# Kernel tuning notes

Hardware: AMD Instinct MI355X
Metric: run time of the kernel (lower is better)

Reference implementation:

```python
import jax, jax.numpy as jnp
import numpy as np

B, N, E, G, V = 8, 512, 8192, 1024, 100000
HD, FIN, BN_EPS = 1024, 20, 1e-5


def setup_inputs() -> dict:
    key = jax.random.key(0)
    ks = jax.random.split(key, 8)
    return {
        'h': jax.random.normal(ks[0], (B, N, FIN), jnp.float32),
        'src': jax.random.randint(ks[1], (B, E), 0, N, jnp.int32),
        'dst': jax.random.randint(ks[2], (B, E), 0, N, jnp.int32),
        'gPos': jax.random.randint(ks[3], (B, G), 0, V, jnp.int32),
        'allDBGEmb': jax.random.normal(ks[4], (V, HD), jnp.float32),
        'fc_init_w': jax.random.normal(ks[5], (HD, FIN), jnp.float32) * (1.0 / np.sqrt(FIN)),
        'fc_init_b': jnp.zeros((HD,), jnp.float32),
        'bn1_g': jnp.ones((HD,), jnp.float32),
        'bn1_b': jnp.zeros((HD,), jnp.float32),
        'bn2_g': jnp.ones((HD,), jnp.float32),
        'bn2_b': jnp.zeros((HD,), jnp.float32),
        'fc_w': jax.random.normal(ks[6], (128, 2 * HD), jnp.float32) * (1.0 / np.sqrt(2 * HD)),
        'fc_b': jnp.zeros((128,), jnp.float32),
        'bn3_g': jnp.ones((128,), jnp.float32),
        'bn3_b': jnp.zeros((128,), jnp.float32),
        'fc2_w': jax.random.normal(ks[7], (1, 128), jnp.float32) * (1.0 / np.sqrt(128)),
        'fc2_b': jnp.zeros((1,), jnp.float32),
    }


def _bn(x, g, b):
    # BatchNorm1d in training mode: batch statistics over axis 0 (biased var)
    mu = x.mean(0)
    var = ((x - mu) ** 2).mean(0)
    return (x - mu) * jax.lax.rsqrt(var + BN_EPS) * g + b


def _gin_mean(x, s, d):
    # GINConv(None, 'mean') with eps=0: h_v + mean_{u in N(v)} h_u
    sums = jax.ops.segment_sum(x[s], d, num_segments=N)  # [N, HD]
    deg = jax.ops.segment_sum(jnp.ones((E, 1), x.dtype), d, num_segments=N)
    return x + jnp.where(deg > 0, sums / jnp.maximum(deg, 1.0), 0.0)


def reference(h, src, dst, gPos, allDBGEmb, fc_init_w, fc_init_b,
              bn1_g, bn1_b, bn2_g, bn2_b, fc_w, fc_b, bn3_g, bn3_b,
              fc2_w, fc2_b):
    def per_graph(hq, s, d, gp):
        x = hq @ fc_init_w.T + fc_init_b                      # [N, HD]
        x = jax.nn.relu(_bn(_gin_mean(x, s, d), bn1_g, bn1_b))
        x = jax.nn.relu(_bn(_gin_mean(x, s, d), bn2_g, bn2_b))
        qemb = x.mean(0)                                      # dgl.mean_nodes
        gEmb = allDBGEmb[gp]                                  # [G, HD]
        H = jnp.concatenate([jnp.broadcast_to(qemb, (G, HD)), gEmb], axis=1)
        h2 = jax.nn.relu(_bn(H @ fc_w.T + fc_b, bn3_g, bn3_b))
        return jax.nn.sigmoid(h2 @ fc2_w.T + fc2_b).reshape(-1)  # [G]

    return jax.vmap(per_graph)(h, src, dst, gPos)  # [B, G]
```

## Files before the change

### kernel.cpp

```cpp
#include <hip/hip_runtime.h>
#include <hip/hip_bf16.h>

#define B_ 8
#define G_ 1024
#define HD_ 1024
#define EPS_ 1e-5f


typedef __attribute__((ext_vector_type(8))) short bf16x8;
typedef __attribute__((ext_vector_type(4))) float f32x4;

__device__ inline short bf1(float x) {
    return (short)__builtin_bit_cast(unsigned short, __float2bfloat16(x));
}
__device__ inline bf16x8 cvt8(float4 a, float4 b) {
    bf16x8 o;
    o[0] = bf1(a.x); o[1] = bf1(a.y); o[2] = bf1(a.z); o[3] = bf1(a.w);
    o[4] = bf1(b.x); o[5] = bf1(b.y); o[6] = bf1(b.z); o[7] = bf1(b.w);
    return o;
}

__global__ __launch_bounds__(256) void k_w2cvt(const float* __restrict__ fc_w,
                                               short* __restrict__ w2arr) {
    int gid = blockIdx.x * 256 + threadIdx.x;
    int kt = gid >> 9;
    int jblk = (gid >> 6) & 7;
    int lane = gid & 63;
    int j = jblk * 16 + (lane & 15);
    int k = kt * 32 + (lane >> 4) * 8;
    const float4* sp = (const float4*)&fc_w[(size_t)j * (2 * HD_) + HD_ + k];
    *(bf16x8*)&w2arr[(size_t)gid * 8] = cvt8(sp[0], sp[1]);
}

#define ASLAB 258

__global__ __launch_bounds__(512) void k_gemm(const int* __restrict__ gPos,
                                              const float* __restrict__ emb,
                                              const short* __restrict__ w2arr,
                                              float* __restrict__ z,
                                              float* __restrict__ ps,
                                              float* __restrict__ pq) {
    int b = blockIdx.y, gblk = blockIdx.x;
    int gbase = gblk * 32;
    int tid = threadIdx.x;
    int wave = tid >> 6, lane = tid & 63;
    int gq = wave >> 2, jq = wave & 3;
    int l15 = lane & 15, kb = lane >> 4;

    __shared__ int gidx[32];
    __shared__ short As[2][16 * ASLAB];

    if (tid < 32) gidx[tid] = gPos[b * G_ + gbase + tid];
    __syncthreads();

    int arow = tid >> 4, acp = tid & 15;
    const float* abase = emb + (size_t)gidx[arow] * HD_;

    f32x4 acc0 = {0.f, 0.f, 0.f, 0.f}, acc1 = {0.f, 0.f, 0.f, 0.f};

    {
        const float4* ap = (const float4*)(abase + acp * 8);
        *(bf16x8*)&As[0][acp * ASLAB + arow * 8] = cvt8(ap[0], ap[1]);
    }
    __syncthreads();

    for (int p = 0; p < 8; ++p) {
        int cur = p & 1;
        if (p < 7) {
            const float4* ap = (const float4*)(abase + (p + 1) * 128 + acp * 8);
            *(bf16x8*)&As[cur ^ 1][acp * ASLAB + arow * 8] = cvt8(ap[0], ap[1]);
        }
#pragma unroll
        for (int kt = 0; kt < 4; ++kt) {
            bf16x8 a = *(const bf16x8*)&As[cur][(kt * 4 + kb) * ASLAB + (gq * 16 + l15) * 8];
            int f = (p * 4 + kt) * 8 + jq * 2;
            bf16x8 b0 = *(const bf16x8*)&w2arr[((size_t)f * 64 + lane) * 8];
            bf16x8 b1 = *(const bf16x8*)&w2arr[((size_t)(f + 1) * 64 + lane) * 8];
            acc0 = __builtin_amdgcn_mfma_f32_16x16x32_bf16(a, b0, acc0, 0, 0, 0);
            acc1 = __builtin_amdgcn_mfma_f32_16x16x32_bf16(a, b1, acc1, 0, 0, 0);
        }
        __syncthreads();
    }

    int col0 = jq * 32 + l15, col1 = col0 + 16;
    float s0 = 0.f, q0 = 0.f, s1 = 0.f, q1 = 0.f;
#pragma unroll
    for (int r = 0; r < 4; ++r) {
        int g = gbase + gq * 16 + kb * 4 + r;
        float z0 = acc0[r], z1 = acc1[r];
        z[(size_t)(b * G_ + g) * 128 + col0] = z0;
        z[(size_t)(b * G_ + g) * 128 + col1] = z1;
        s0 += z0; q0 += z0 * z0;
        s1 += z1; q1 += z1 * z1;
    }
    s0 += __shfl_xor(s0, 16, 64); s0 += __shfl_xor(s0, 32, 64);
    q0 += __shfl_xor(q0, 16, 64); q0 += __shfl_xor(q0, 32, 64);
    s1 += __shfl_xor(s1, 16, 64); s1 += __shfl_xor(s1, 32, 64);
    q1 += __shfl_xor(q1, 16, 64); q1 += __shfl_xor(q1, 32, 64);
    if (lane < 16) {
        int slot = (b * 64 + gblk * 2 + gq) * 128;
        ps[slot + col0] = s0; pq[slot + col0] = q0;
        ps[slot + col1] = s1; pq[slot + col1] = q1;
    }
}

__global__ void k_stats(const float* __restrict__ ps, const float* __restrict__ pq,
                        const float* __restrict__ g3, const float* __restrict__ b3,
                        float* __restrict__ scv, float* __restrict__ shv) {
    int b = blockIdx.x, j = threadIdx.x;
    float s = 0.f, q = 0.f;
#pragma unroll 8
    for (int t = 0; t < 64; ++t) {
        s += ps[(b * 64 + t) * 128 + j];
        q += pq[(b * 64 + t) * 128 + j];
    }
    float mu = s * (1.f / G_);
    float var = q * (1.f / G_) - mu * mu;
    float sc = g3[j] * rsqrtf(var + EPS_);
    scv[b * 128 + j] = sc;
    shv[b * 128 + j] = b3[j] - mu * sc;
}

__global__ __launch_bounds__(256) void k_final(const float* __restrict__ z,
                                               const float* __restrict__ scv,
                                               const float* __restrict__ shv,
                                               const float* __restrict__ fc2w,
                                               const float* __restrict__ fc2b,
                                               float* __restrict__ out) {
    int wid = (blockIdx.x * blockDim.x + threadIdx.x) >> 6;
    int lane = threadIdx.x & 63;
    int b = wid >> 10;
    const float* zr = z + (size_t)wid * 128;
    float acc = 0.f;
#pragma unroll
    for (int t = 0; t < 2; ++t) {
        int j = lane + t * 64;
        float v = fmaf(zr[j], scv[b * 128 + j], shv[b * 128 + j]);
        v = fmaxf(v, 0.f);
        acc += v * fc2w[j];
    }
    for (int off = 32; off; off >>= 1) acc += __shfl_down(acc, off, 64);
    if (lane == 0) out[wid] = 1.f / (1.f + expf(-(acc + fc2b[0])));
}

extern "C" void kernel_launch(void* const* d_in, const int* in_sizes, int n_in,
                              void* d_out, int out_size, void* d_ws, size_t ws_size,
                              hipStream_t stream) {
    const int*   gPos = (const int*)d_in[3];
    const float* emb  = (const float*)d_in[4];
    const float* fc_w = (const float*)d_in[11];
    const float* bn3g = (const float*)d_in[13];
    const float* bn3b = (const float*)d_in[14];
    const float* fc2w = (const float*)d_in[15];
    const float* fc2b = (const float*)d_in[16];
    float* out = (float*)d_out;

    char* w = (char*)d_ws;
    float* z     = (float*)w; w += (size_t)B_ * G_ * 128 * 4;
    short* w2arr = (short*)w; w += (size_t)128 * HD_ * 2;
    float* ps    = (float*)w; w += (size_t)B_ * 64 * 128 * 4;
    float* pq    = (float*)w; w += (size_t)B_ * 64 * 128 * 4;
    float* scv   = (float*)w; w += (size_t)B_ * 128 * 4;
    float* shv   = (float*)w; w += (size_t)B_ * 128 * 4;

    k_w2cvt<<<64, 256, 0, stream>>>(fc_w, w2arr);
    k_gemm<<<dim3(32, B_), 512, 0, stream>>>(gPos, emb, w2arr, z, ps, pq);
    k_stats<<<B_, 128, 0, stream>>>(ps, pq, bn3g, bn3b, scv, shv);
    k_final<<<(B_ * G_) / 4, 256, 0, stream>>>(z, scv, shv, fc2w, fc2b, out);
}
```

Measured before the change: 28.97 us.

## Halve GEMM row tile to 16 rows per block, doubling grid to 512 blocks

The gather-GEMM block now handles 16 gathered embedding rows instead of 32. Each of its 8 waves computes one 16-column output slice with a single accumulator, and each thread loads one float4 per stage instead of two. The grid doubles to 64x8 blocks so more CUs can pull the random embedding rows at once, which targets the latency-bound gather. The cost is that each block reuses the weight fragments over half as many rows, so B-operand traffic from L2 doubles.

```diff
diff --git a/kernel.cpp b/kernel.cpp
--- a/kernel.cpp
+++ b/kernel.cpp
@@ -8,6 +8,7 @@
 
 
 typedef __attribute__((ext_vector_type(8))) short bf16x8;
+typedef __attribute__((ext_vector_type(4))) short bf16x4;
 typedef __attribute__((ext_vector_type(4))) float f32x4;
 
 __device__ inline short bf1(float x) {
@@ -17,6 +18,11 @@
     bf16x8 o;
     o[0] = bf1(a.x); o[1] = bf1(a.y); o[2] = bf1(a.z); o[3] = bf1(a.w);
     o[4] = bf1(b.x); o[5] = bf1(b.y); o[6] = bf1(b.z); o[7] = bf1(b.w);
+    return o;
+}
+__device__ inline bf16x4 cvt4(float4 a) {
+    bf16x4 o;
+    o[0] = bf1(a.x); o[1] = bf1(a.y); o[2] = bf1(a.z); o[3] = bf1(a.w);
     return o;
 }
 
@@ -32,7 +38,7 @@
     *(bf16x8*)&w2arr[(size_t)gid * 8] = cvt8(sp[0], sp[1]);
 }
 
-#define ASLAB 258
+#define SLAB16 130
 
 __global__ __launch_bounds__(512) void k_gemm(const int* __restrict__ gPos,
                                               const float* __restrict__ emb,
@@ -41,66 +47,60 @@
                                               float* __restrict__ ps,
                                               float* __restrict__ pq) {
     int b = blockIdx.y, gblk = blockIdx.x;
-    int gbase = gblk * 32;
+    int gbase = gblk * 16;
     int tid = threadIdx.x;
-    int wave = tid >> 6, lane = tid & 63;
-    int gq = wave >> 2, jq = wave & 3;
+    int jq = tid >> 6, lane = tid & 63;
     int l15 = lane & 15, kb = lane >> 4;
 
-    __shared__ int gidx[32];
-    __shared__ short As[2][16 * ASLAB];
+    __shared__ int gidx[16];
+    __shared__ short As[2][16 * SLAB16];
 
-    if (tid < 32) gidx[tid] = gPos[b * G_ + gbase + tid];
+    if (tid < 16) gidx[tid] = gPos[b * G_ + gbase + tid];
     __syncthreads();
 
-    int arow = tid >> 4, acp = tid & 15;
+    int arow = tid >> 5, acp = tid & 31;
     const float* abase = emb + (size_t)gidx[arow] * HD_;
+    int aoff = (acp >> 1) * SLAB16 + arow * 8 + (acp & 1) * 4;
 
-    f32x4 acc0 = {0.f, 0.f, 0.f, 0.f}, acc1 = {0.f, 0.f, 0.f, 0.f};
+    f32x4 acc = {0.f, 0.f, 0.f, 0.f};
 
     {
-        const float4* ap = (const float4*)(abase + acp * 8);
-        *(bf16x8*)&As[0][acp * ASLAB + arow * 8] = cvt8(ap[0], ap[1]);
+        float4 av = *(const float4*)(abase + acp * 4);
+        *(bf16x4*)&As[0][aoff] = cvt4(av);
     }
     __syncthreads();
 
     for (int p = 0; p < 8; ++p) {
         int cur = p & 1;
         if (p < 7) {
-            const float4* ap = (const float4*)(abase + (p + 1) * 128 + acp * 8);
-            *(bf16x8*)&As[cur ^ 1][acp * ASLAB + arow * 8] = cvt8(ap[0], ap[1]);
+            float4 av = *(const float4*)(abase + (p + 1) * 128 + acp * 4);
+            *(bf16x4*)&As[cur ^ 1][aoff] = cvt4(av);
         }
 #pragma unroll
         for (int kt = 0; kt < 4; ++kt) {
-            bf16x8 a = *(const bf16x8*)&As[cur][(kt * 4 + kb) * ASLAB + (gq * 16 + l15) * 8];
-            int f = (p * 4 + kt) * 8 + jq * 2;
-            bf16x8 b0 = *(const bf16x8*)&w2arr[((size_t)f * 64 + lane) * 8];
-            bf16x8 b1 = *(const bf16x8*)&w2arr[((size_t)(f + 1) * 64 + lane) * 8];
-            acc0 = __builtin_amdgcn_mfma_f32_16x16x32_bf16(a, b0, acc0, 0, 0, 0);
-            acc1 = __builtin_amdgcn_mfma_f32_16x16x32_bf16(a, b1, acc1, 0, 0, 0);
+            int f = (p * 4 + kt) * 8 + jq;
+            bf16x8 bv = *(const bf16x8*)&w2arr[((size_t)f * 64 + lane) * 8];
+            bf16x8 a = *(const bf16x8*)&As[cur][(kt * 4 + kb) * SLAB16 + l15 * 8];
+            acc = __builtin_amdgcn_mfma_f32_16x16x32_bf16(a, bv, acc, 0, 0, 0);
         }
         __syncthreads();
     }
 
-    int col0 = jq * 32 + l15, col1 = col0 + 16;
-    float s0 = 0.f, q0 = 0.f, s1 = 0.f, q1 = 0.f;
+    int jcol = jq * 16 + l15;
+    float s = 0.f, q = 0.f;
 #pragma unroll
     for (int r = 0; r < 4; ++r) {
-        int g = gbase + gq * 16 + kb * 4 + r;
-        float z0 = acc0[r], z1 = acc1[r];
-        z[(size_t)(b * G_ + g) * 128 + col0] = z0;
-        z[(size_t)(b * G_ + g) * 128 + col1] = z1;
-        s0 += z0; q0 += z0 * z0;
-        s1 += z1; q1 += z1 * z1;
+        float v = acc[r];
+        int g = gbase + kb * 4 + r;
+        z[(size_t)(b * G_ + g) * 128 + jcol] = v;
+        s += v;
+        q += v * v;
     }
-    s0 += __shfl_xor(s0, 16, 64); s0 += __shfl_xor(s0, 32, 64);
-    q0 += __shfl_xor(q0, 16, 64); q0 += __shfl_xor(q0, 32, 64);
-    s1 += __shfl_xor(s1, 16, 64); s1 += __shfl_xor(s1, 32, 64);
-    q1 += __shfl_xor(q1, 16, 64); q1 += __shfl_xor(q1, 32, 64);
+    s += __shfl_xor(s, 16, 64); s += __shfl_xor(s, 32, 64);
+    q += __shfl_xor(q, 16, 64); q += __shfl_xor(q, 32, 64);
     if (lane < 16) {
-        int slot = (b * 64 + gblk * 2 + gq) * 128;
-        ps[slot + col0] = s0; pq[slot + col0] = q0;
-        ps[slot + col1] = s1; pq[slot + col1] = q1;
+        ps[(b * 64 + gblk) * 128 + jcol] = s;
+        pq[(b * 64 + gblk) * 128 + jcol] = q;
     }
 }
 
@@ -164,7 +164,7 @@
     float* shv   = (float*)w; w += (size_t)B_ * 128 * 4;
 
     k_w2cvt<<<64, 256, 0, stream>>>(fc_w, w2arr);
-    k_gemm<<<dim3(32, B_), 512, 0, stream>>>(gPos, emb, w2arr, z, ps, pq);
+    k_gemm<<<dim3(64, B_), 512, 0, stream>>>(gPos, emb, w2arr, z, ps, pq);
     k_stats<<<B_, 128, 0, stream>>>(ps, pq, bn3g, bn3b, scv, shv);
     k_final<<<(B_ * G_) / 4, 256, 0, stream>>>(z, scv, shv, fc2w, fc2b, out);
 }
```

New measurement: 27.19 us (median of 2 runs). 1.07x faster.
